# Performance work log

Hardware: AMD Instinct MI355X
Metric: run time of the kernel (lower is better)

Reference implementation:

```python
import jax, jax.numpy as jnp
import numpy as np

B, S, D, H = 4, 2048, 1024, 16
HS = D // H  # head_size = 64


def setup_inputs() -> dict:
    key = jax.random.key(0)
    ks = jax.random.split(key, 6)
    scale = 0.02
    return {
        "token_embeddings": jax.random.normal(ks[0], (B, S, D), dtype=jnp.float32),
        # per-head projection weights, stacked: [H, D, HS] (x @ W per head)
        "Wq": jax.random.normal(ks[1], (H, D, HS), dtype=jnp.float32) * scale,
        "Wk": jax.random.normal(ks[2], (H, D, HS), dtype=jnp.float32) * scale,
        "Wv": jax.random.normal(ks[3], (H, D, HS), dtype=jnp.float32) * scale,
        # output projection (Linear with bias): y = x @ Wo + bo
        "Wo": jax.random.normal(ks[4], (D, D), dtype=jnp.float32) * scale,
        "bo": jax.random.normal(ks[5], (D,), dtype=jnp.float32) * scale,
    }


def reference(token_embeddings, Wq, Wk, Wv, Wo, bo):
    # Per-head projections, batched over heads: [B,H,S,HS]
    q = jnp.einsum("bsd,hde->bhse", token_embeddings, Wq)
    k = jnp.einsum("bsd,hde->bhse", token_embeddings, Wk)
    v = jnp.einsum("bsd,hde->bhse", token_embeddings, Wv)
    scale = HS ** -0.5
    scores = jnp.einsum("bhqe,bhke->bhqk", q, k) * scale  # [B,H,S,S]
    causal = jnp.tril(jnp.ones((S, S), dtype=bool))
    scores = jnp.where(causal, scores, -jnp.inf)
    weights = jax.nn.softmax(scores, axis=-1)
    # dropout in eval mode -> identity
    out = jnp.einsum("bhqk,bhke->bhqe", weights, v)  # [B,H,S,HS]
    # concat heads -> [B,S,D] (head order matches torch.cat over heads)
    out = out.transpose(0, 2, 1, 3).reshape(B, S, D)
    return out @ Wo + bo
```

## Files before the change

kernel.cpp:

```cpp
#include <hip/hip_runtime.h>


typedef __bf16 bf16;
typedef bf16 bf16x8 __attribute__((ext_vector_type(8)));
typedef bf16 bf16x4 __attribute__((ext_vector_type(4)));
typedef float f32x4 __attribute__((ext_vector_type(4)));

__device__ __forceinline__ void gload16(const void* gsrc, void* ldst) {
  __builtin_amdgcn_global_load_lds(
      (const __attribute__((address_space(1))) unsigned int*)gsrc,
      (__attribute__((address_space(3))) unsigned int*)ldst, 16, 0, 0);
}

__device__ __forceinline__ f32x4 mfma16(bf16x8 a, bf16x8 b, f32x4 c) {
  return __builtin_amdgcn_mfma_f32_16x16x32_bf16(a, b, c, 0, 0, 0);
}

__global__ __launch_bounds__(256) void pack_x_kernel(const float* __restrict__ x,
                                                     bf16* __restrict__ xb) {
  int i = (blockIdx.x * 256 + threadIdx.x) * 4;
  float4 v = *(const float4*)(x + i);
  bf16x4 o;
  o[0] = (bf16)v.x; o[1] = (bf16)v.y; o[2] = (bf16)v.z; o[3] = (bf16)v.w;
  *(bf16x4*)(xb + i) = o;
}

__global__ __launch_bounds__(256) void pack_wqkv_kernel(const float* __restrict__ Wq,
                                                        const float* __restrict__ Wk,
                                                        const float* __restrict__ Wv,
                                                        bf16* __restrict__ WT) {
  int idx = blockIdx.x * 256 + threadIdx.x;
  int n = idx >> 10, k = idx & 1023;
  int sel = n >> 10, nn = n & 1023;
  const float* W = (sel == 0) ? Wq : (sel == 1 ? Wk : Wv);
  int h = nn >> 6, e = nn & 63;
  WT[(size_t)n * 1024 + k] = (bf16)W[h * 65536 + k * 64 + e];
}

__global__ __launch_bounds__(256) void pack_wo_kernel(const float* __restrict__ Wo,
                                                      bf16* __restrict__ WoT) {
  int idx = blockIdx.x * 256 + threadIdx.x;
  int n = idx >> 10, k = idx & 1023;
  WoT[idx] = (bf16)Wo[k * 1024 + n];
}

template <bool F32OUT>
__global__ __launch_bounds__(256) void gemm_bt_kernel(const bf16* __restrict__ A,
                                                      const bf16* __restrict__ BT,
                                                      bf16* __restrict__ Cb,
                                                      float* __restrict__ Cf,
                                                      const float* __restrict__ bias,
                                                      int M, int N, int K) {
  __shared__ bf16 As[128 * 32];
  __shared__ bf16 Bs[128 * 32];
  const int tid = threadIdx.x, lane = tid & 63, wave = tid >> 6;
  const int g = lane >> 4, c = lane & 15;
  const int nx = gridDim.x;
  const int nwg = nx * gridDim.y;
  const int bid = blockIdx.y * nx + blockIdx.x;
  const int swz = (bid & 7) * (nwg >> 3) + (bid >> 3);
  const int m0 = (swz / nx) * 128, n0 = (swz % nx) * 128;
  const int wr = wave >> 1, wc = wave & 1;

  f32x4 acc[4][4] = {};
  for (int k0 = 0; k0 < K; k0 += 32) {
#pragma unroll
    for (int t = 0; t < 2; ++t) {
      int o = t * 4096 + wave * 1024 + lane * 16;
      int row = o >> 6, kb = (o & 63) >> 1;
      gload16(A + (size_t)(m0 + row) * K + k0 + kb, (char*)As + o);
      gload16(BT + (size_t)(n0 + row) * K + k0 + kb, (char*)Bs + o);
    }
    __syncthreads();
    bf16x8 af[4], bfr[4];
#pragma unroll
    for (int m = 0; m < 4; ++m)
      af[m] = *(const bf16x8*)((const char*)As + (wr * 64 + m * 16 + c) * 64 + g * 16);
#pragma unroll
    for (int n = 0; n < 4; ++n)
      bfr[n] = *(const bf16x8*)((const char*)Bs + (wc * 64 + n * 16 + c) * 64 + g * 16);
#pragma unroll
    for (int m = 0; m < 4; ++m)
#pragma unroll
      for (int n = 0; n < 4; ++n)
        acc[m][n] = mfma16(af[m], bfr[n], acc[m][n]);
    __syncthreads();
  }
#pragma unroll
  for (int m = 0; m < 4; ++m)
#pragma unroll
    for (int n = 0; n < 4; ++n)
#pragma unroll
      for (int i = 0; i < 4; ++i) {
        int row = m0 + wr * 64 + m * 16 + g * 4 + i;
        int col = n0 + wc * 64 + n * 16 + c;
        if (F32OUT)
          Cf[(size_t)row * N + col] = acc[m][n][i] + bias[col];
        else
          Cb[(size_t)row * N + col] = (bf16)acc[m][n][i];
      }
}

__global__ __launch_bounds__(256) void transpose_v_kernel(const bf16* __restrict__ qkv,
                                                          bf16* __restrict__ vt) {
  __shared__ bf16 tl[64][72];
  const int tid = threadIdx.x;
  const int st = blockIdx.x, bh = blockIdx.y;
  const int b = bh >> 4, h = bh & 15;
#pragma unroll
  for (int it = 0; it < 2; ++it) {
    int idx = it * 256 + tid;
    int sl = idx >> 3, ch = idx & 7;
    bf16x8 v = *(const bf16x8*)(qkv + (size_t)(b * 2048 + st * 64 + sl) * 3072 + 2048 + h * 64 + ch * 8);
    *(bf16x8*)&tl[sl][ch * 8] = v;
  }
  __syncthreads();
#pragma unroll
  for (int it = 0; it < 2; ++it) {
    int idx = it * 256 + tid;
    int d = idx >> 3, s8 = idx & 7;
    bf16x8 o;
#pragma unroll
    for (int j = 0; j < 8; ++j) o[j] = tl[s8 * 8 + j][d];
    *(bf16x8*)(vt + ((size_t)bh * 64 + d) * 2048 + st * 64 + s8 * 8) = o;
  }
}

__global__ __launch_bounds__(512, 4) void attn_kernel(const bf16* __restrict__ qkv,
                                                      const bf16* __restrict__ vt,
                                                      bf16* __restrict__ attn_out) {
  __shared__ bf16 Ks[2][128 * 64];
  __shared__ bf16 Vs[2][64 * 128];
  const int tid = threadIdx.x, lane = tid & 63, wave = tid >> 6;
  const int g = lane >> 4, c = lane & 15;
  const int bid = blockIdx.x;
  const int xcd = bid & 7;
  const int x = (bid >> 3) & 7;
  const int bh = (bid >> 6) * 8 + xcd;
  const int b = bh >> 4, h = bh & 15;
  const float SCL = 0.125f * 1.4426950408889634f;

  bf16x8 ones;
#pragma unroll
  for (int j = 0; j < 8; ++j) ones[j] = (bf16)1.0f;

#define STAGE(KT, BUF)                                                                    \
  do {                                                                                    \
    _Pragma("unroll") for (int t2 = 0; t2 < 2; ++t2) {                                    \
      int o = t2 * 8192 + wave * 1024 + lane * 16;                          \
      int rK = o >> 7, chK = (((o & 127) >> 4) ^ (rK & 7));                               \
      gload16((const char*)qkv +                                                          \
                  ((size_t)(b * 2048 + (KT)*128 + rK) * 3072 + 1024 + h * 64) * 2 +       \
                  (chK << 4),                                                             \
              (char*)Ks[BUF] + o);                                                        \
      int rV = o >> 8, chV = (((o & 255) >> 4) ^ (rV & 7));                               \
      gload16((const char*)vt + (((size_t)bh * 64 + rV) * 2048 + (KT)*128) * 2 +          \
                  (chV << 4),                                                             \
              (char*)Vs[BUF] + o);                                                        \
    }                                                                                     \
  } while (0)

#pragma unroll 1
  for (int ph = 0; ph < 2; ++ph) {
    const int qt = ph ? (15 - x) : x;
    const int qlow = qt * 128 + wave * 16;

    bf16x8 qf[2];
#pragma unroll
    for (int kk = 0; kk < 2; ++kk) {
      size_t row = (size_t)(b * 2048 + qlow + c);
      qf[kk] = *(const bf16x8*)(qkv + row * 3072 + h * 64 + kk * 32 + g * 8);
    }

    f32x4 oacc[4] = {};
    f32x4 lacc = {};
    float mrun = -3.0e38f;

    const int nkt = qt + 1;
    STAGE(0, 0);
    for (int kt = 0; kt < nkt; ++kt) {
      const int cur = kt & 1;
      if (kt + 1 < nkt) {
        STAGE(kt + 1, cur ^ 1);
        asm volatile("s_waitcnt vmcnt(4)" ::: "memory");
      } else {
        asm volatile("s_waitcnt vmcnt(0)" ::: "memory");
      }
      __builtin_amdgcn_sched_barrier(0);
      __builtin_amdgcn_s_barrier();
      __builtin_amdgcn_sched_barrier(0);
      f32x4 sc[8] = {};
      __builtin_amdgcn_s_setprio(1);
#pragma unroll
      for (int n = 0; n < 8; ++n) {
        int key = n * 16 + c;
#pragma unroll
        for (int kk = 0; kk < 2; ++kk) {
          bf16x8 kf = *(const bf16x8*)((const char*)Ks[cur] + key * 128 +
                                       (((kk * 4 + g) ^ (key & 7)) << 4));
          sc[n] = mfma16(kf, qf[kk], sc[n]);
        }
      }
      __builtin_amdgcn_s_setprio(0);
      const int q = qlow + c;
      if (kt == qt) {
#pragma unroll
        for (int n = 0; n < 8; ++n)
#pragma unroll
          for (int i = 0; i < 4; ++i)
            sc[n][i] = ((kt * 128 + n * 16 + 4 * g + i) <= q) ? sc[n][i] : -3.0e38f;
      }
      float vmax = -3.0e38f;
#pragma unroll
      for (int n = 0; n < 8; ++n)
#pragma unroll
        for (int i = 0; i < 4; ++i) vmax = fmaxf(vmax, sc[n][i]);
      vmax = fmaxf(vmax, __shfl_xor(vmax, 16));
      vmax = fmaxf(vmax, __shfl_xor(vmax, 32));
      const float mnew = fmaxf(mrun, vmax * SCL);
      const float fs = __builtin_amdgcn_exp2f(mrun - mnew);
      mrun = mnew;
#pragma unroll
      for (int n = 0; n < 8; ++n)
#pragma unroll
        for (int i = 0; i < 4; ++i)
          sc[n][i] = __builtin_amdgcn_exp2f(fmaf(sc[n][i], SCL, -mnew));
#pragma unroll
      for (int i = 0; i < 4; ++i) {
        float fsb = __shfl(fs, ((lane >> 4) << 2) + i);
        lacc[i] *= fsb;
#pragma unroll
        for (int dn = 0; dn < 4; ++dn) oacc[dn][i] *= fsb;
      }
      bf16x8 pa[4];
#pragma unroll
      for (int kss = 0; kss < 4; ++kss) {
        bf16x8 t;
#pragma unroll
        for (int j = 0; j < 4; ++j) t[j] = (bf16)sc[2 * kss][j];
#pragma unroll
        for (int j = 0; j < 4; ++j) t[4 + j] = (bf16)sc[2 * kss + 1][j];
        pa[kss] = t;
      }
      __builtin_amdgcn_s_setprio(1);
#pragma unroll
      for (int kss = 0; kss < 4; ++kss) {
        lacc = mfma16(pa[kss], ones, lacc);
#pragma unroll
        for (int dn = 0; dn < 4; ++dn) {
          const int d = dn * 16 + c;
          const char* vrow = (const char*)Vs[cur] + d * 256;
          const int off = 8 * (g & 1);
          bf16x4 lo = *(const bf16x4*)(vrow + (((4 * kss + (g >> 1)) ^ (d & 7)) << 4) + off);
          bf16x4 hi = *(const bf16x4*)(vrow + (((4 * kss + 2 + (g >> 1)) ^ (d & 7)) << 4) + off);
          bf16x8 vb;
#pragma unroll
          for (int j = 0; j < 4; ++j) { vb[j] = lo[j]; vb[4 + j] = hi[j]; }
          oacc[dn] = mfma16(pa[kss], vb, oacc[dn]);
        }
      }
      __builtin_amdgcn_s_setprio(0);
      __builtin_amdgcn_sched_barrier(0);
      __builtin_amdgcn_s_barrier();
      __builtin_amdgcn_sched_barrier(0);
    }
#pragma unroll
    for (int i = 0; i < 4; ++i) {
      float inv = __builtin_amdgcn_rcpf(lacc[i]);
      size_t row = (size_t)(b * 2048 + qlow + 4 * g + i);
#pragma unroll
      for (int dn = 0; dn < 4; ++dn)
        attn_out[row * 1024 + h * 64 + dn * 16 + c] = (bf16)(oacc[dn][i] * inv);
    }
  }
#undef STAGE
}

extern "C" void kernel_launch(void* const* d_in, const int* in_sizes, int n_in,
                              void* d_out, int out_size, void* d_ws, size_t ws_size,
                              hipStream_t stream) {
  const float* x  = (const float*)d_in[0];
  const float* Wq = (const float*)d_in[1];
  const float* Wk = (const float*)d_in[2];
  const float* Wv = (const float*)d_in[3];
  const float* Wo = (const float*)d_in[4];
  const float* bo = (const float*)d_in[5];
  float* out = (float*)d_out;
  char* ws = (char*)d_ws;

  bf16* Xb    = (bf16*)(ws);
  bf16* WqkvT = (bf16*)(ws + 16777216);
  bf16* WoT   = (bf16*)(ws + 23068672);
  bf16* QKV   = (bf16*)(ws + 25165824);
  bf16* VT    = (bf16*)(ws + 75497472);
  bf16* AttnO = (bf16*)(ws + 92274688);

  pack_x_kernel<<<8192, 256, 0, stream>>>(x, Xb);
  pack_wqkv_kernel<<<12288, 256, 0, stream>>>(Wq, Wk, Wv, WqkvT);
  pack_wo_kernel<<<4096, 256, 0, stream>>>(Wo, WoT);
  gemm_bt_kernel<false><<<dim3(24, 64), 256, 0, stream>>>(Xb, WqkvT, QKV, nullptr, nullptr,
                                                          8192, 3072, 1024);
  transpose_v_kernel<<<dim3(32, 64), 256, 0, stream>>>(QKV, VT);
  attn_kernel<<<512, 512, 0, stream>>>(QKV, VT, AttnO);
  gemm_bt_kernel<true><<<dim3(8, 64), 256, 0, stream>>>(AttnO, WoT, nullptr, out, bo,
                                                        8192, 1024, 1024);
}
```

Before: 197.4 us.

## Pipeline GEMM with multi-stage async LDS loads, swizzled LDS, and 8-wave blocks

Replaces the synchronous single-buffered GEMM with a four-stage software pipeline that issues global-to-LDS loads three K-steps ahead and waits with explicit vmcnt counters. LDS chunks are XOR-swizzled to cut bank conflicts, blocks grow to 512 threads (8 waves, each covering a 64x32 tile), and setprio is raised around the MFMA section. The goal is to hide global load latency and drop one barrier per K-step, at the cost of more LDS per block, hardcoded K=1024 loop bounds, and fragile hand-written wait counts.

New measurement: 196.2 us. Within noise of the previous version (-0.6%).

```diff
diff --git a/kernel.cpp b/kernel.cpp
--- a/kernel.cpp
+++ b/kernel.cpp
@@ -45,55 +45,87 @@
 }
 
 template <bool F32OUT>
-__global__ __launch_bounds__(256) void gemm_bt_kernel(const bf16* __restrict__ A,
-                                                      const bf16* __restrict__ BT,
-                                                      bf16* __restrict__ Cb,
-                                                      float* __restrict__ Cf,
-                                                      const float* __restrict__ bias,
-                                                      int M, int N, int K) {
-  __shared__ bf16 As[128 * 32];
-  __shared__ bf16 Bs[128 * 32];
+__global__ __launch_bounds__(512, 4) void gemm3_kernel(const bf16* __restrict__ A,
+                                                       const bf16* __restrict__ BT,
+                                                       bf16* __restrict__ Cb,
+                                                       float* __restrict__ Cf,
+                                                       const float* __restrict__ bias,
+                                                       int N, int K, int NT) {
+  __shared__ bf16 As[2][2][128 * 32];
+  __shared__ bf16 Bs[2][2][128 * 32];
   const int tid = threadIdx.x, lane = tid & 63, wave = tid >> 6;
   const int g = lane >> 4, c = lane & 15;
-  const int nx = gridDim.x;
-  const int nwg = nx * gridDim.y;
-  const int bid = blockIdx.y * nx + blockIdx.x;
-  const int swz = (bid & 7) * (nwg >> 3) + (bid >> 3);
-  const int m0 = (swz / nx) * 128, n0 = (swz % nx) * 128;
-  const int wr = wave >> 1, wc = wave & 1;
-
-  f32x4 acc[4][4] = {};
-  for (int k0 = 0; k0 < K; k0 += 32) {
-#pragma unroll
-    for (int t = 0; t < 2; ++t) {
-      int o = t * 4096 + wave * 1024 + lane * 16;
-      int row = o >> 6, kb = (o & 63) >> 1;
-      gload16(A + (size_t)(m0 + row) * K + k0 + kb, (char*)As + o);
-      gload16(BT + (size_t)(n0 + row) * K + k0 + kb, (char*)Bs + o);
-    }
-    __syncthreads();
-    bf16x8 af[4], bfr[4];
+  const int wr = wave >> 2, wc = wave & 3;
+  const int bid = blockIdx.x;
+  const int q8 = gridDim.x >> 3;
+  const int swz = (bid & 7) * q8 + (bid >> 3);
+  const int m0 = (swz / NT) * 128, n0 = (swz % NT) * 128;
+
+  const int r_s = tid >> 2;
+  const int chs = (tid & 3) ^ ((r_s >> 1) & 3);
+  const int chsw = (g ^ ((c >> 1) & 3)) << 4;
+
+#define STAGE3(P)                                                                   \
+  do {                                                                             \
+    const int t_ = (P) >> 1, kh_ = (P)&1, bf_ = t_ & 1;                            \
+    const int kofs = t_ * 64 + kh_ * 32 + chs * 8;                                 \
+    gload16(A + (size_t)(m0 + r_s) * K + kofs, (char*)&As[bf_][kh_][0] + tid * 16); \
+    gload16(BT + (size_t)(n0 + r_s) * K + kofs, (char*)&Bs[bf_][kh_][0] + tid * 16); \
+  } while (0)
+
+  f32x4 acc[4][2] = {};
+  STAGE3(0);
+  STAGE3(1);
+  STAGE3(2);
+  asm volatile("s_waitcnt vmcnt(4)" ::: "memory");
+  __builtin_amdgcn_sched_barrier(0);
+  __builtin_amdgcn_s_barrier();
+  __builtin_amdgcn_sched_barrier(0);
+
+#pragma unroll 1
+  for (int p = 0; p < 32; ++p) {
+    if (p <= 28) STAGE3(p + 3);
+    const char* abase = (const char*)&As[(p >> 1) & 1][p & 1][0];
+    const char* bbase = (const char*)&Bs[(p >> 1) & 1][p & 1][0];
+    bf16x8 af[4], bfr[2];
 #pragma unroll
     for (int m = 0; m < 4; ++m)
-      af[m] = *(const bf16x8*)((const char*)As + (wr * 64 + m * 16 + c) * 64 + g * 16);
-#pragma unroll
-    for (int n = 0; n < 4; ++n)
-      bfr[n] = *(const bf16x8*)((const char*)Bs + (wc * 64 + n * 16 + c) * 64 + g * 16);
+      af[m] = *(const bf16x8*)(abase + (wr * 64 + m * 16 + c) * 64 + chsw);
+#pragma unroll
+    for (int n = 0; n < 2; ++n)
+      bfr[n] = *(const bf16x8*)(bbase + (wc * 32 + n * 16 + c) * 64 + chsw);
+    asm volatile("s_waitcnt lgkmcnt(0)" ::: "memory");
+    __builtin_amdgcn_sched_barrier(0);
+    __builtin_amdgcn_s_setprio(1);
 #pragma unroll
     for (int m = 0; m < 4; ++m)
 #pragma unroll
-      for (int n = 0; n < 4; ++n)
+      for (int n = 0; n < 2; ++n)
         acc[m][n] = mfma16(af[m], bfr[n], acc[m][n]);
-    __syncthreads();
+    __builtin_amdgcn_s_setprio(0);
+    __builtin_amdgcn_sched_barrier(0);
+    if (p <= 28) {
+      asm volatile("s_waitcnt vmcnt(4)" ::: "memory");
+    } else if (p == 29) {
+      asm volatile("s_waitcnt vmcnt(2)" ::: "memory");
+    } else if (p == 30) {
+      asm volatile("s_waitcnt vmcnt(0)" ::: "memory");
+    }
+    if (p < 31) {
+      __builtin_amdgcn_sched_barrier(0);
+      __builtin_amdgcn_s_barrier();
+      __builtin_amdgcn_sched_barrier(0);
+    }
   }
+#undef STAGE3
 #pragma unroll
   for (int m = 0; m < 4; ++m)
 #pragma unroll
-    for (int n = 0; n < 4; ++n)
+    for (int n = 0; n < 2; ++n)
 #pragma unroll
       for (int i = 0; i < 4; ++i) {
         int row = m0 + wr * 64 + m * 16 + g * 4 + i;
-        int col = n0 + wc * 64 + n * 16 + c;
+        int col = n0 + wc * 32 + n * 16 + c;
         if (F32OUT)
           Cf[(size_t)row * N + col] = acc[m][n][i] + bias[col];
         else
@@ -298,10 +330,10 @@
   pack_x_kernel<<<8192, 256, 0, stream>>>(x, Xb);
   pack_wqkv_kernel<<<12288, 256, 0, stream>>>(Wq, Wk, Wv, WqkvT);
   pack_wo_kernel<<<4096, 256, 0, stream>>>(Wo, WoT);
-  gemm_bt_kernel<false><<<dim3(24, 64), 256, 0, stream>>>(Xb, WqkvT, QKV, nullptr, nullptr,
-                                                          8192, 3072, 1024);
+  gemm3_kernel<false><<<1536, 512, 0, stream>>>(Xb, WqkvT, QKV, nullptr, nullptr,
+                                                3072, 1024, 24);
   transpose_v_kernel<<<dim3(32, 64), 256, 0, stream>>>(QKV, VT);
   attn_kernel<<<512, 512, 0, stream>>>(QKV, VT, AttnO);
-  gemm_bt_kernel<true><<<dim3(8, 64), 256, 0, stream>>>(AttnO, WoT, nullptr, out, bo,
-                                                        8192, 1024, 1024);
-}
+  gemm3_kernel<true><<<512, 512, 0, stream>>>(AttnO, WoT, nullptr, out, bo,
+                                              1024, 1024, 8);
+}
```

## Rewrite projection GEMMs with double-buffered swizzled LDS and XCD-aware tile mapping

Applied to the files above, without the earlier changes.

Replaces the single-buffered GEMM (K-step 32) with a double-buffered version that uses a K-step of 64. The next tile is prefetched while MFMAs run on the current one, leaving one barrier per step instead of two. LDS rows are XOR-swizzled to avoid bank conflicts, and blocks are mapped so that each XCD gets a contiguous group of M tiles for L2 reuse. MFMA priority is raised during the compute phase. LDS use grows to 64KB per block, which can limit occupancy, and the tile mapping assumes M=8192 with exactly 8 XCDs.

Measured after the change: 181.7 us. 7.9% less time.

```diff
diff --git a/kernel.cpp b/kernel.cpp
--- a/kernel.cpp
+++ b/kernel.cpp
@@ -45,47 +45,85 @@
 }
 
 template <bool F32OUT>
-__global__ __launch_bounds__(256) void gemm_bt_kernel(const bf16* __restrict__ A,
-                                                      const bf16* __restrict__ BT,
-                                                      bf16* __restrict__ Cb,
-                                                      float* __restrict__ Cf,
-                                                      const float* __restrict__ bias,
-                                                      int M, int N, int K) {
-  __shared__ bf16 As[128 * 32];
-  __shared__ bf16 Bs[128 * 32];
+__global__ __launch_bounds__(256, 2) void gemm4_kernel(const bf16* __restrict__ A,
+                                                       const bf16* __restrict__ BT,
+                                                       bf16* __restrict__ Cb,
+                                                       float* __restrict__ Cf,
+                                                       const float* __restrict__ bias,
+                                                       int N, int K) {
+  __shared__ bf16 As[2][128 * 64];
+  __shared__ bf16 Bs[2][128 * 64];
   const int tid = threadIdx.x, lane = tid & 63, wave = tid >> 6;
   const int g = lane >> 4, c = lane & 15;
-  const int nx = gridDim.x;
-  const int nwg = nx * gridDim.y;
-  const int bid = blockIdx.y * nx + blockIdx.x;
-  const int swz = (bid & 7) * (nwg >> 3) + (bid >> 3);
-  const int m0 = (swz / nx) * 128, n0 = (swz % nx) * 128;
   const int wr = wave >> 1, wc = wave & 1;
+  const int bid = blockIdx.x;
+  const int xcd = bid & 7, local = bid >> 3;
+  const int m0 = (xcd * 8 + (local & 7)) * 128;
+  const int n0 = (local >> 3) * 128;
+
+  const int schunk = (lane & 7) ^ (lane >> 3);
+
+#define STAGE4(T, S)                                                      \
+  do {                                                                    \
+    _Pragma("unroll") for (int j = 0; j < 4; ++j) {                       \
+      const int r = wave * 32 + j * 8 + (lane >> 3);                      \
+      const int ldso = wave * 4096 + j * 1024 + lane * 16;                \
+      gload16(A + (size_t)(m0 + r) * K + (T)*64 + schunk * 8,             \
+              (char*)&As[S][0] + ldso);                                   \
+      gload16(BT + (size_t)(n0 + r) * K + (T)*64 + schunk * 8,            \
+              (char*)&Bs[S][0] + ldso);                                   \
+    }                                                                     \
+  } while (0)
 
   f32x4 acc[4][4] = {};
-  for (int k0 = 0; k0 < K; k0 += 32) {
-#pragma unroll
-    for (int t = 0; t < 2; ++t) {
-      int o = t * 4096 + wave * 1024 + lane * 16;
-      int row = o >> 6, kb = (o & 63) >> 1;
-      gload16(A + (size_t)(m0 + row) * K + k0 + kb, (char*)As + o);
-      gload16(BT + (size_t)(n0 + row) * K + k0 + kb, (char*)Bs + o);
-    }
-    __syncthreads();
-    bf16x8 af[4], bfr[4];
-#pragma unroll
-    for (int m = 0; m < 4; ++m)
-      af[m] = *(const bf16x8*)((const char*)As + (wr * 64 + m * 16 + c) * 64 + g * 16);
-#pragma unroll
-    for (int n = 0; n < 4; ++n)
-      bfr[n] = *(const bf16x8*)((const char*)Bs + (wc * 64 + n * 16 + c) * 64 + g * 16);
-#pragma unroll
-    for (int m = 0; m < 4; ++m)
-#pragma unroll
-      for (int n = 0; n < 4; ++n)
-        acc[m][n] = mfma16(af[m], bfr[n], acc[m][n]);
-    __syncthreads();
+  const int nt = K >> 6;
+  STAGE4(0, 0);
+  asm volatile("s_waitcnt vmcnt(0)" ::: "memory");
+  __builtin_amdgcn_sched_barrier(0);
+  __builtin_amdgcn_s_barrier();
+  __builtin_amdgcn_sched_barrier(0);
+
+#pragma unroll 1
+  for (int t = 0; t < nt; ++t) {
+    const int s = t & 1;
+    if (t + 1 < nt) STAGE4(t + 1, s ^ 1);
+    bf16x8 af[4][2], bfr[4][2];
+#pragma unroll
+    for (int m = 0; m < 4; ++m) {
+      const int row = wr * 64 + m * 16 + c;
+#pragma unroll
+      for (int kk = 0; kk < 2; ++kk)
+        af[m][kk] = *(const bf16x8*)((const char*)&As[s][0] + row * 128 +
+                                     (((kk * 4 + g) ^ (row & 7)) << 4));
+    }
+#pragma unroll
+    for (int n = 0; n < 4; ++n) {
+      const int row = wc * 64 + n * 16 + c;
+#pragma unroll
+      for (int kk = 0; kk < 2; ++kk)
+        bfr[n][kk] = *(const bf16x8*)((const char*)&Bs[s][0] + row * 128 +
+                                      (((kk * 4 + g) ^ (row & 7)) << 4));
+    }
+    asm volatile("s_waitcnt lgkmcnt(0)" ::: "memory");
+    __builtin_amdgcn_sched_barrier(0);
+    __builtin_amdgcn_s_setprio(1);
+#pragma unroll
+    for (int kk = 0; kk < 2; ++kk)
+#pragma unroll
+      for (int m = 0; m < 4; ++m)
+#pragma unroll
+        for (int n = 0; n < 4; ++n)
+          acc[m][n] = mfma16(af[m][kk], bfr[n][kk], acc[m][n]);
+    __builtin_amdgcn_s_setprio(0);
+    __builtin_amdgcn_sched_barrier(0);
+    if (t + 1 < nt) {
+      asm volatile("s_waitcnt vmcnt(0)" ::: "memory");
+      __builtin_amdgcn_sched_barrier(0);
+      __builtin_amdgcn_s_barrier();
+      __builtin_amdgcn_sched_barrier(0);
+    }
   }
+#undef STAGE4
 #pragma unroll
   for (int m = 0; m < 4; ++m)
 #pragma unroll
@@ -298,10 +336,10 @@
   pack_x_kernel<<<8192, 256, 0, stream>>>(x, Xb);
   pack_wqkv_kernel<<<12288, 256, 0, stream>>>(Wq, Wk, Wv, WqkvT);
   pack_wo_kernel<<<4096, 256, 0, stream>>>(Wo, WoT);
-  gemm_bt_kernel<false><<<dim3(24, 64), 256, 0, stream>>>(Xb, WqkvT, QKV, nullptr, nullptr,
-                                                          8192, 3072, 1024);
+  gemm4_kernel<false><<<1536, 256, 0, stream>>>(Xb, WqkvT, QKV, nullptr, nullptr,
+                                                3072, 1024);
   transpose_v_kernel<<<dim3(32, 64), 256, 0, stream>>>(QKV, VT);
   attn_kernel<<<512, 512, 0, stream>>>(QKV, VT, AttnO);
-  gemm_bt_kernel<true><<<dim3(8, 64), 256, 0, stream>>>(AttnO, WoT, nullptr, out, bo,
-                                                        8192, 1024, 1024);
-}
+  gemm4_kernel<true><<<512, 256, 0, stream>>>(AttnO, WoT, nullptr, out, bo,
+                                              1024, 1024);
+}
```
